# Kernel tuning notes

Measured on AMD Instinct MI355X. Metric: run time of the kernel, lower is better.

## Reference

```python
import jax, jax.numpy as jnp
import numpy as np

N_NODES = 50000
N_EDGES = 600000
IN_DIM = 128
HID = 256
OUT = 3


def setup_inputs() -> dict:
    key = jax.random.key(0)
    ks = jax.random.split(key, 10)
    x = jax.random.normal(ks[0], (N_NODES, IN_DIM), dtype=jnp.float32)
    edge_index = jax.random.randint(ks[1], (2, N_EDGES), 0, N_NODES, dtype=jnp.int64)
    s = lambda k, shp: jax.random.normal(k, shp, dtype=jnp.float32) * (1.0 / np.sqrt(shp[0]))
    return {
        "x": x,
        "edge_index": edge_index,
        # SAGEConv1: lin_l (applied to aggregated neighbors, with bias), lin_r (root, no bias)
        "W1l": s(ks[2], (IN_DIM, HID)), "b1": jnp.zeros((HID,), jnp.float32), "W1r": s(ks[3], (IN_DIM, HID)),
        # SAGEConv2
        "W2l": s(ks[4], (HID, HID)), "b2": jnp.zeros((HID,), jnp.float32), "W2r": s(ks[5], (HID, HID)),
        # classification head
        "Wh": s(ks[6], (HID, OUT)), "bh": jnp.zeros((OUT,), jnp.float32),
    }


def _sage_conv(x, edge_index, Wl, b, Wr):
    """PyG SAGEConv with mean aggregation: out = lin_l(mean_{j->i} x_j) + lin_r(x_i)."""
    src, dst = edge_index[0], edge_index[1]
    n = x.shape[0]
    # gather source features and scatter-mean onto targets
    msg_sum = jax.ops.segment_sum(x[src], dst, num_segments=n)          # [N, d]
    deg = jax.ops.segment_sum(jnp.ones((src.shape[0],), x.dtype), dst, num_segments=n)
    mean = msg_sum / jnp.maximum(deg, 1.0)[:, None]                      # isolated nodes -> 0
    return mean @ Wl + b + x @ Wr


def reference(x, edge_index, W1l, b1, W1r, W2l, b2, W2r, Wh, bh):
    h = jax.nn.relu(_sage_conv(x, edge_index, W1l, b1, W1r))
    # dropout(p=0.2) is identity in eval mode
    h = jax.nn.relu(_sage_conv(h, edge_index, W2l, b2, W2r))
    return h @ Wh + bh
```

## Files before the change

### kernel.cpp

```cpp
#include <hip/hip_runtime.h>
#include <hip/hip_bf16.h>

#define N_NODES 50000
#define N_EDGES 600000
#define IN_DIM 128
#define HID 256
#define OUT_DIM 3

#define M_PAD 50048

#define SCAN_B 256
#define SCAN_NB ((N_NODES + SCAN_B - 1) / SCAN_B)

typedef __bf16 bf16x8 __attribute__((ext_vector_type(8)));
typedef float f32x4 __attribute__((ext_vector_type(4)));

static __device__ __forceinline__ unsigned short f2b(float f) {
    union { float f; unsigned u; } u; u.f = f;
    unsigned r = u.u + 0x7fffu + ((u.u >> 16) & 1u);
    return (unsigned short)(r >> 16);
}
static __device__ __forceinline__ float b2f(unsigned short b) {
    union { unsigned u; float f; } u; u.u = ((unsigned)b) << 16;
    return u.f;
}

static __device__ __forceinline__ size_t swz(int r, int k, int K) {
    return (((size_t)((r >> 4) * (K >> 5) + (k >> 5))) << 9)
         + ((((k >> 3) & 3) * 16 + (r & 15)) << 3) + (k & 7);
}


__global__ void count_deg_kernel(const int* __restrict__ dst, int* __restrict__ counts) {
    int e = blockIdx.x * blockDim.x + threadIdx.x;
    if (e < N_EDGES) atomicAdd(&counts[dst[e]], 1);
}

__global__ __launch_bounds__(256) void block_sum_kernel(const int* __restrict__ counts,
                                                        int* __restrict__ partial) {
    int node = blockIdx.x * SCAN_B + threadIdx.x;
    int v = (node < N_NODES) ? counts[node] : 0;
#pragma unroll
    for (int off = 32; off > 0; off >>= 1) v += __shfl_down(v, off);
    __shared__ int ws[4];
    if ((threadIdx.x & 63) == 0) ws[threadIdx.x >> 6] = v;
    __syncthreads();
    if (threadIdx.x == 0) partial[blockIdx.x] = ws[0] + ws[1] + ws[2] + ws[3];
}

__global__ __launch_bounds__(256) void scan_partial_kernel(int* __restrict__ partial) {
    __shared__ int s[SCAN_B];
    int t = threadIdx.x;
    int v = (t < SCAN_NB) ? partial[t] : 0;
    s[t] = v;
    __syncthreads();
    for (int off = 1; off < SCAN_B; off <<= 1) {
        int u = (t >= off) ? s[t - off] : 0;
        __syncthreads();
        s[t] += u;
        __syncthreads();
    }
    if (t < SCAN_NB) partial[t] = s[t] - v;
}

__global__ __launch_bounds__(256) void write_rowptr_kernel(const int* __restrict__ counts,
                                                           const int* __restrict__ partial,
                                                           int* __restrict__ row_ptr) {
    __shared__ int s[SCAN_B];
    int t = threadIdx.x;
    int node = blockIdx.x * SCAN_B + t;
    int v = (node < N_NODES) ? counts[node] : 0;
    s[t] = v;
    __syncthreads();
    for (int off = 1; off < SCAN_B; off <<= 1) {
        int u = (t >= off) ? s[t - off] : 0;
        __syncthreads();
        s[t] += u;
        __syncthreads();
    }
    if (node < N_NODES) row_ptr[node] = partial[blockIdx.x] + s[t] - v;
    if (node == 0) row_ptr[N_NODES] = N_EDGES;
}

__global__ void fill_csr_kernel(const int* __restrict__ src, const int* __restrict__ dst,
                                const int* __restrict__ row_ptr, int* __restrict__ cursor,
                                int* __restrict__ csr_src) {
    int e = blockIdx.x * blockDim.x + threadIdx.x;
    if (e < N_EDGES) {
        int d = dst[e];
        int pos = atomicAdd(&cursor[d], 1);
        csr_src[row_ptr[d] + pos] = src[e];
    }
}


__global__ void cast_f2b_kernel(const float* __restrict__ in,
                                unsigned short* __restrict__ out_row,
                                unsigned short* __restrict__ out_swz) {
    int i = blockIdx.x * blockDim.x + threadIdx.x;
    if (i * 4 < N_NODES * IN_DIM) {
        float4 v = ((const float4*)in)[i];
        ushort4 o;
        o.x = f2b(v.x); o.y = f2b(v.y); o.z = f2b(v.z); o.w = f2b(v.w);
        ((ushort4*)out_row)[i] = o;
        int m = i >> 5;
        int kb = (i & 31) * 4;
        *(ushort4*)(out_swz + swz(m, kb, IN_DIM)) = o;
    }
}

__global__ void tcast4_kernel(const float* __restrict__ W1l, const float* __restrict__ W1r,
                              const float* __restrict__ W2l, const float* __restrict__ W2r,
                              unsigned short* __restrict__ W1lt, unsigned short* __restrict__ W1rt,
                              unsigned short* __restrict__ W2lt, unsigned short* __restrict__ W2rt) {
    int i = blockIdx.x * blockDim.x + threadIdx.x;
    const float* in; unsigned short* out; int K, base;
    if (i < 32768)        { in = W1l; out = W1lt; K = IN_DIM; base = 0; }
    else if (i < 65536)   { in = W1r; out = W1rt; K = IN_DIM; base = 32768; }
    else if (i < 131072)  { in = W2l; out = W2lt; K = HID;    base = 65536; }
    else if (i < 196608)  { in = W2r; out = W2rt; K = HID;    base = 131072; }
    else return;
    int j = i - base;
    int k = j >> 8;
    int n = j & 255;
    out[swz(n, k, K)] = f2b(in[j]);
}

__global__ void init_out_kernel(const float* __restrict__ bh, float* __restrict__ out) {
    int i = blockIdx.x * blockDim.x + threadIdx.x;
    if (i < N_NODES * 3) out[i] = bh[i % 3];
}


static __device__ __forceinline__ void addv(float* acc, uint4 v) {
    acc[0] += b2f((unsigned short)(v.x & 0xffff));
    acc[1] += b2f((unsigned short)(v.x >> 16));
    acc[2] += b2f((unsigned short)(v.y & 0xffff));
    acc[3] += b2f((unsigned short)(v.y >> 16));
    acc[4] += b2f((unsigned short)(v.z & 0xffff));
    acc[5] += b2f((unsigned short)(v.z >> 16));
    acc[6] += b2f((unsigned short)(v.w & 0xffff));
    acc[7] += b2f((unsigned short)(v.w >> 16));
}

static __device__ __forceinline__ uint4 pack8(const float* a) {
    uint4 pk;
    pk.x = (unsigned)f2b(a[0]) | ((unsigned)f2b(a[1]) << 16);
    pk.y = (unsigned)f2b(a[2]) | ((unsigned)f2b(a[3]) << 16);
    pk.z = (unsigned)f2b(a[4]) | ((unsigned)f2b(a[5]) << 16);
    pk.w = (unsigned)f2b(a[6]) | ((unsigned)f2b(a[7]) << 16);
    return pk;
}

__global__ __launch_bounds__(256) void agg_mean256_kernel(const unsigned short* __restrict__ feat,
                                                          const int* __restrict__ row_ptr,
                                                          const int* __restrict__ csr_src,
                                                          unsigned short* __restrict__ out_swz) {
    int node = blockIdx.x * 4 + (threadIdx.x >> 6);
    if (node >= N_NODES) return;
    int lane = threadIdx.x & 63;
    int half = lane >> 5, lh = lane & 31;
    const uint4* f4 = (const uint4*)feat;
    float acc[8];
#pragma unroll
    for (int j = 0; j < 8; j++) acc[j] = 0.f;
    int beg = row_ptr[node], end = row_ptr[node + 1];
    int i = beg;
    for (; i + 4 <= end; i += 4) {
        int sA = csr_src[i + half];
        int sB = csr_src[i + 2 + half];
        uint4 vA = f4[(size_t)sA * 32 + lh];
        uint4 vB = f4[(size_t)sB * 32 + lh];
        addv(acc, vA);
        addv(acc, vB);
    }
    if (i + 2 <= end) {
        int s = csr_src[i + half];
        addv(acc, f4[(size_t)s * 32 + lh]);
        i += 2;
    }
    if (i < end && half == 0) {
        int s = csr_src[i];
        addv(acc, f4[(size_t)s * 32 + lh]);
    }
    float inv = (end > beg) ? 1.0f / (float)(end - beg) : 0.0f;
#pragma unroll
    for (int j = 0; j < 8; j++) {
        acc[j] += __shfl_xor(acc[j], 32);
        acc[j] *= inv;
    }
    if (half == 0) *(uint4*)(out_swz + swz(node, lh * 8, HID)) = pack8(acc);
}

__global__ __launch_bounds__(256) void agg_mean128_kernel(const unsigned short* __restrict__ feat,
                                                          const int* __restrict__ row_ptr,
                                                          const int* __restrict__ csr_src,
                                                          unsigned short* __restrict__ out_swz) {
    int node = blockIdx.x * 4 + (threadIdx.x >> 6);
    if (node >= N_NODES) return;
    int lane = threadIdx.x & 63;
    int q = lane >> 4, lq = lane & 15;
    const uint4* f4 = (const uint4*)feat;
    float acc[8];
#pragma unroll
    for (int j = 0; j < 8; j++) acc[j] = 0.f;
    int beg = row_ptr[node], end = row_ptr[node + 1];
    int i = beg;
    for (; i + 8 <= end; i += 8) {
        int sA = csr_src[i + q];
        int sB = csr_src[i + 4 + q];
        uint4 vA = f4[(size_t)sA * 16 + lq];
        uint4 vB = f4[(size_t)sB * 16 + lq];
        addv(acc, vA);
        addv(acc, vB);
    }
    if (i + 4 <= end) {
        int s = csr_src[i + q];
        addv(acc, f4[(size_t)s * 16 + lq]);
        i += 4;
    }
    int rem = end - i;
    if (q < rem) {
        int s = csr_src[i + q];
        addv(acc, f4[(size_t)s * 16 + lq]);
    }
    float inv = (end > beg) ? 1.0f / (float)(end - beg) : 0.0f;
#pragma unroll
    for (int j = 0; j < 8; j++) {
        acc[j] += __shfl_xor(acc[j], 32);
        acc[j] += __shfl_xor(acc[j], 16);
        acc[j] *= inv;
    }
    if (q == 0) *(uint4*)(out_swz + swz(node, lq * 8, IN_DIM)) = pack8(acc);
}


template <int K>
static __device__ __forceinline__ void gemm_swz_core(
    const unsigned short* __restrict__ A0, const unsigned short* __restrict__ B0,
    const unsigned short* __restrict__ A1, const unsigned short* __restrict__ B1,
    int tmw, int tn0, int l, f32x4 (&acc)[2][8]) {
    constexpr int KT = K / 32;
    const unsigned short* Ap[2] = {A0, A1};
    const unsigned short* Bp[2] = {B0, B1};
#pragma unroll
    for (int p = 0; p < 2; p++) {
        const unsigned short* A = Ap[p];
        const unsigned short* B = Bp[p];
#pragma unroll
        for (int tk = 0; tk < KT; tk++) {
            bf16x8 a[2], b[8];
            a[0] = *(const bf16x8*)(A + ((((size_t)tmw) * KT + tk) << 9) + l * 8);
            a[1] = *(const bf16x8*)(A + ((((size_t)tmw + 1) * KT + tk) << 9) + l * 8);
#pragma unroll
            for (int nt = 0; nt < 8; nt++)
                b[nt] = *(const bf16x8*)(B + ((((size_t)tn0 + nt) * KT + tk) << 9) + l * 8);
#pragma unroll
            for (int mt = 0; mt < 2; mt++)
#pragma unroll
                for (int nt = 0; nt < 8; nt++)
                    acc[mt][nt] = __builtin_amdgcn_mfma_f32_16x16x32_bf16(a[mt], b[nt],
                                                                          acc[mt][nt], 0, 0, 0);
        }
    }
}

template <int K>
__global__ __launch_bounds__(256, 3) void gemm_swz_kernel(
    const unsigned short* __restrict__ A0, const unsigned short* __restrict__ B0,
    const unsigned short* __restrict__ A1, const unsigned short* __restrict__ B1,
    const float* __restrict__ bias, unsigned short* __restrict__ out_row,
    unsigned short* __restrict__ out_swz, int M) {
    const int t = threadIdx.x;
    const int w = t >> 6, l = t & 63;
    const int quad = l >> 4, lr = l & 15;
    const int m0 = blockIdx.x * 128, n0 = blockIdx.y * 128;
    const int tmw = (m0 >> 4) + w * 2, tn0 = n0 >> 4;

    f32x4 acc[2][8];
    const f32x4 zero = {0.f, 0.f, 0.f, 0.f};
#pragma unroll
    for (int mt = 0; mt < 2; mt++)
#pragma unroll
        for (int nt = 0; nt < 8; nt++) acc[mt][nt] = zero;

    float bias_r[8];
#pragma unroll
    for (int nt = 0; nt < 8; nt++) bias_r[nt] = bias[n0 + nt * 16 + lr];

    gemm_swz_core<K>(A0, B0, A1, B1, tmw, tn0, l, acc);

#pragma unroll
    for (int mt = 0; mt < 2; mt++)
#pragma unroll
        for (int r = 0; r < 4; r++) {
            int gm = m0 + w * 32 + mt * 16 + quad * 4 + r;
            if (gm >= M) continue;
            unsigned short* orow = out_row + (size_t)gm * HID;
#pragma unroll
            for (int nt = 0; nt < 8; nt++) {
                int gn = n0 + nt * 16 + lr;
                unsigned short h = f2b(fmaxf(acc[mt][nt][r] + bias_r[nt], 0.f));
                orow[gn] = h;
                out_swz[swz(gm, gn, HID)] = h;
            }
        }
}

template <int K>
__global__ __launch_bounds__(256, 3) void gemm_swz_head_kernel(
    const unsigned short* __restrict__ A0, const unsigned short* __restrict__ B0,
    const unsigned short* __restrict__ A1, const unsigned short* __restrict__ B1,
    const float* __restrict__ bias, const float* __restrict__ Wh,
    float* __restrict__ out, int M) {
    const int t = threadIdx.x;
    const int w = t >> 6, l = t & 63;
    const int quad = l >> 4, lr = l & 15;
    const int m0 = blockIdx.x * 128, n0 = blockIdx.y * 128;
    const int tmw = (m0 >> 4) + w * 2, tn0 = n0 >> 4;

    f32x4 acc[2][8];
    const f32x4 zero = {0.f, 0.f, 0.f, 0.f};
#pragma unroll
    for (int mt = 0; mt < 2; mt++)
#pragma unroll
        for (int nt = 0; nt < 8; nt++) acc[mt][nt] = zero;

    float bias_r[8];
    float wh_r[8][3];
#pragma unroll
    for (int nt = 0; nt < 8; nt++) {
        int gn = n0 + nt * 16 + lr;
        bias_r[nt] = bias[gn];
        wh_r[nt][0] = Wh[gn * 3 + 0];
        wh_r[nt][1] = Wh[gn * 3 + 1];
        wh_r[nt][2] = Wh[gn * 3 + 2];
    }

    gemm_swz_core<K>(A0, B0, A1, B1, tmw, tn0, l, acc);

#pragma unroll
    for (int mt = 0; mt < 2; mt++)
#pragma unroll
        for (int r = 0; r < 4; r++) {
            int gm = m0 + w * 32 + mt * 16 + quad * 4 + r;
            float p0 = 0.f, p1 = 0.f, p2 = 0.f;
#pragma unroll
            for (int nt = 0; nt < 8; nt++) {
                float v = fmaxf(acc[mt][nt][r] + bias_r[nt], 0.f);
                p0 += v * wh_r[nt][0];
                p1 += v * wh_r[nt][1];
                p2 += v * wh_r[nt][2];
            }
#pragma unroll
            for (int off = 1; off < 16; off <<= 1) {
                p0 += __shfl_xor(p0, off);
                p1 += __shfl_xor(p1, off);
                p2 += __shfl_xor(p2, off);
            }
            if (lr == 0 && gm < M) {
                atomicAdd(&out[(size_t)gm * 3 + 0], p0);
                atomicAdd(&out[(size_t)gm * 3 + 1], p1);
                atomicAdd(&out[(size_t)gm * 3 + 2], p2);
            }
        }
}


extern "C" void kernel_launch(void* const* d_in, const int* in_sizes, int n_in,
                              void* d_out, int out_size, void* d_ws, size_t ws_size,
                              hipStream_t stream) {
    const float* x   = (const float*)d_in[0];
    const int*   ei  = (const int*)d_in[1];
    const int*   src = ei;
    const int*   dst = ei + N_EDGES;
    const float* W1l = (const float*)d_in[2];
    const float* b1  = (const float*)d_in[3];
    const float* W1r = (const float*)d_in[4];
    const float* W2l = (const float*)d_in[5];
    const float* b2  = (const float*)d_in[6];
    const float* W2r = (const float*)d_in[7];
    const float* Wh  = (const float*)d_in[8];
    const float* bh  = (const float*)d_in[9];
    float* out = (float*)d_out;

    char* ws = (char*)d_ws;
    size_t off = 0;
    auto alloc = [&](size_t bytes) -> void* {
        void* p = ws + off;
        off = (off + bytes + 255) & ~(size_t)255;
        return p;
    };
    int* counts   = (int*)alloc((size_t)N_NODES * 4);
    int* row_ptr  = (int*)alloc((size_t)(N_NODES + 1) * 4);
    int* cursor   = (int*)alloc((size_t)N_NODES * 4);
    int* partial  = (int*)alloc((size_t)SCAN_NB * 4);
    int* csr_src  = (int*)alloc((size_t)N_EDGES * 4);
    unsigned short* xb_row  = (unsigned short*)alloc((size_t)M_PAD * IN_DIM * 2);
    unsigned short* xb_swz  = (unsigned short*)alloc((size_t)M_PAD * IN_DIM * 2);
    unsigned short* agg1    = (unsigned short*)alloc((size_t)M_PAD * IN_DIM * 2);
    unsigned short* h1_row  = (unsigned short*)alloc((size_t)M_PAD * HID * 2);
    unsigned short* h1_swz  = (unsigned short*)alloc((size_t)M_PAD * HID * 2);
    unsigned short* agg2    = (unsigned short*)alloc((size_t)M_PAD * HID * 2);
    unsigned short* W1lt = (unsigned short*)alloc((size_t)IN_DIM * HID * 2);
    unsigned short* W1rt = (unsigned short*)alloc((size_t)IN_DIM * HID * 2);
    unsigned short* W2lt = (unsigned short*)alloc((size_t)HID * HID * 2);
    unsigned short* W2rt = (unsigned short*)alloc((size_t)HID * HID * 2);

    hipMemsetAsync(counts, 0, (size_t)N_NODES * 4, stream);
    hipMemsetAsync(cursor, 0, (size_t)N_NODES * 4, stream);

    const int eblocks = (N_EDGES + 255) / 256;
    count_deg_kernel<<<eblocks, 256, 0, stream>>>(dst, counts);
    block_sum_kernel<<<SCAN_NB, SCAN_B, 0, stream>>>(counts, partial);
    scan_partial_kernel<<<1, SCAN_B, 0, stream>>>(partial);
    write_rowptr_kernel<<<SCAN_NB, SCAN_B, 0, stream>>>(counts, partial, row_ptr);
    fill_csr_kernel<<<eblocks, 256, 0, stream>>>(src, dst, row_ptr, cursor, csr_src);

    {
        int n = N_NODES * IN_DIM;
        cast_f2b_kernel<<<(n / 4 + 255) / 256, 256, 0, stream>>>(x, xb_row, xb_swz);
        tcast4_kernel<<<(196608 + 255) / 256, 256, 0, stream>>>(W1l, W1r, W2l, W2r,
                                                                W1lt, W1rt, W2lt, W2rt);
        init_out_kernel<<<(N_NODES * 3 + 255) / 256, 256, 0, stream>>>(bh, out);
    }

    const int nblocks4 = (N_NODES + 3) / 4;
    dim3 gg(M_PAD / 128, 2);

    agg_mean128_kernel<<<nblocks4, 256, 0, stream>>>(xb_row, row_ptr, csr_src, agg1);
    gemm_swz_kernel<IN_DIM><<<gg, 256, 0, stream>>>(agg1, W1lt, xb_swz, W1rt, b1,
                                                    h1_row, h1_swz, N_NODES);

    agg_mean256_kernel<<<nblocks4, 256, 0, stream>>>(h1_row, row_ptr, csr_src, agg2);
    gemm_swz_head_kernel<HID><<<gg, 256, 0, stream>>>(agg2, W2lt, h1_swz, W2rt, b2, Wh,
                                                      out, N_NODES);
}
```

Baseline: 307.9 us.

## Shrink GEMM N-tile to 64, double-buffer register loads, reorder grid for A reuse

Both SAGE GEMM kernels now compute 128x64 output tiles instead of 128x128, which halves the accumulator registers and drops the occupancy hint from launch_bounds. The K loop is flattened across the two operand pairs and software-pipelined: the next k-tile's A/B fragments are loaded into a second register buffer while the MFMAs for the current one run. The grid is transposed so the four N-blocks sharing the same M rows launch next to each other, which should improve L2 reuse of the A tiles. In exchange there are twice as many blocks, each A tile is read four times instead of twice, and the head kernel issues twice as many atomic adds to the output.

```diff
diff --git a/kernel.cpp b/kernel.cpp
--- a/kernel.cpp
+++ b/kernel.cpp
@@ -235,38 +235,44 @@
 }
 
 
-template <int K>
-static __device__ __forceinline__ void gemm_swz_core(
+template <int KP>
+static __device__ __forceinline__ void gemm_swz_core64(
     const unsigned short* __restrict__ A0, const unsigned short* __restrict__ B0,
     const unsigned short* __restrict__ A1, const unsigned short* __restrict__ B1,
-    int tmw, int tn0, int l, f32x4 (&acc)[2][8]) {
-    constexpr int KT = K / 32;
-    const unsigned short* Ap[2] = {A0, A1};
-    const unsigned short* Bp[2] = {B0, B1};
-#pragma unroll
-    for (int p = 0; p < 2; p++) {
-        const unsigned short* A = Ap[p];
-        const unsigned short* B = Bp[p];
-#pragma unroll
-        for (int tk = 0; tk < KT; tk++) {
-            bf16x8 a[2], b[8];
-            a[0] = *(const bf16x8*)(A + ((((size_t)tmw) * KT + tk) << 9) + l * 8);
-            a[1] = *(const bf16x8*)(A + ((((size_t)tmw + 1) * KT + tk) << 9) + l * 8);
-#pragma unroll
-            for (int nt = 0; nt < 8; nt++)
-                b[nt] = *(const bf16x8*)(B + ((((size_t)tn0 + nt) * KT + tk) << 9) + l * 8);
-#pragma unroll
-            for (int mt = 0; mt < 2; mt++)
-#pragma unroll
-                for (int nt = 0; nt < 8; nt++)
-                    acc[mt][nt] = __builtin_amdgcn_mfma_f32_16x16x32_bf16(a[mt], b[nt],
-                                                                          acc[mt][nt], 0, 0, 0);
-        }
-    }
-}
-
-template <int K>
-__global__ __launch_bounds__(256, 3) void gemm_swz_kernel(
+    int tmw, int tn0, int l, f32x4 (&acc)[2][4]) {
+    constexpr int KT = KP / 32;
+    constexpr int TT = 2 * KT;
+    bf16x8 a[2][2], b[2][4];
+
+#define LDTILE(t_, s_)                                                                     \
+    {                                                                                      \
+        const unsigned short* A_ = ((t_) < KT) ? A0 : A1;                                  \
+        const unsigned short* B_ = ((t_) < KT) ? B0 : B1;                                  \
+        const int tk_ = ((t_) < KT) ? (t_) : (t_) - KT;                                    \
+        a[s_][0] = *(const bf16x8*)(A_ + ((((size_t)tmw) * KT + tk_) << 9) + l * 8);       \
+        a[s_][1] = *(const bf16x8*)(A_ + ((((size_t)(tmw + 1)) * KT + tk_) << 9) + l * 8); \
+        _Pragma("unroll")                                                                  \
+        for (int nt = 0; nt < 4; nt++)                                                     \
+            b[s_][nt] = *(const bf16x8*)(B_ + ((((size_t)(tn0 + nt)) * KT + tk_) << 9) + l * 8); \
+    }
+
+    LDTILE(0, 0)
+#pragma unroll
+    for (int t = 0; t < TT; t++) {
+        const int cur = t & 1;
+        if (t + 1 < TT) LDTILE(t + 1, cur ^ 1)
+#pragma unroll
+        for (int mt = 0; mt < 2; mt++)
+#pragma unroll
+            for (int nt = 0; nt < 4; nt++)
+                acc[mt][nt] = __builtin_amdgcn_mfma_f32_16x16x32_bf16(a[cur][mt], b[cur][nt],
+                                                                      acc[mt][nt], 0, 0, 0);
+    }
+#undef LDTILE
+}
+
+template <int KP>
+__global__ __launch_bounds__(256) void gemm_swz_kernel(
     const unsigned short* __restrict__ A0, const unsigned short* __restrict__ B0,
     const unsigned short* __restrict__ A1, const unsigned short* __restrict__ B1,
     const float* __restrict__ bias, unsigned short* __restrict__ out_row,
@@ -274,21 +280,21 @@
     const int t = threadIdx.x;
     const int w = t >> 6, l = t & 63;
     const int quad = l >> 4, lr = l & 15;
-    const int m0 = blockIdx.x * 128, n0 = blockIdx.y * 128;
+    const int n0 = blockIdx.x * 64, m0 = blockIdx.y * 128;
     const int tmw = (m0 >> 4) + w * 2, tn0 = n0 >> 4;
 
-    f32x4 acc[2][8];
+    f32x4 acc[2][4];
     const f32x4 zero = {0.f, 0.f, 0.f, 0.f};
 #pragma unroll
     for (int mt = 0; mt < 2; mt++)
 #pragma unroll
-        for (int nt = 0; nt < 8; nt++) acc[mt][nt] = zero;
-
-    float bias_r[8];
-#pragma unroll
-    for (int nt = 0; nt < 8; nt++) bias_r[nt] = bias[n0 + nt * 16 + lr];
-
-    gemm_swz_core<K>(A0, B0, A1, B1, tmw, tn0, l, acc);
+        for (int nt = 0; nt < 4; nt++) acc[mt][nt] = zero;
+
+    float bias_r[4];
+#pragma unroll
+    for (int nt = 0; nt < 4; nt++) bias_r[nt] = bias[n0 + nt * 16 + lr];
+
+    gemm_swz_core64<KP>(A0, B0, A1, B1, tmw, tn0, l, acc);
 
 #pragma unroll
     for (int mt = 0; mt < 2; mt++)
@@ -298,7 +304,7 @@
             if (gm >= M) continue;
             unsigned short* orow = out_row + (size_t)gm * HID;
 #pragma unroll
-            for (int nt = 0; nt < 8; nt++) {
+            for (int nt = 0; nt < 4; nt++) {
                 int gn = n0 + nt * 16 + lr;
                 unsigned short h = f2b(fmaxf(acc[mt][nt][r] + bias_r[nt], 0.f));
                 orow[gn] = h;
@@ -307,8 +313,8 @@
         }
 }
 
-template <int K>
-__global__ __launch_bounds__(256, 3) void gemm_swz_head_kernel(
+template <int KP>
+__global__ __launch_bounds__(256) void gemm_swz_head_kernel(
     const unsigned short* __restrict__ A0, const unsigned short* __restrict__ B0,
     const unsigned short* __restrict__ A1, const unsigned short* __restrict__ B1,
     const float* __restrict__ bias, const float* __restrict__ Wh,
@@ -316,20 +322,20 @@
     const int t = threadIdx.x;
     const int w = t >> 6, l = t & 63;
     const int quad = l >> 4, lr = l & 15;
-    const int m0 = blockIdx.x * 128, n0 = blockIdx.y * 128;
+    const int n0 = blockIdx.x * 64, m0 = blockIdx.y * 128;
     const int tmw = (m0 >> 4) + w * 2, tn0 = n0 >> 4;
 
-    f32x4 acc[2][8];
+    f32x4 acc[2][4];
     const f32x4 zero = {0.f, 0.f, 0.f, 0.f};
 #pragma unroll
     for (int mt = 0; mt < 2; mt++)
 #pragma unroll
-        for (int nt = 0; nt < 8; nt++) acc[mt][nt] = zero;
-
-    float bias_r[8];
-    float wh_r[8][3];
-#pragma unroll
-    for (int nt = 0; nt < 8; nt++) {
+        for (int nt = 0; nt < 4; nt++) acc[mt][nt] = zero;
+
+    float bias_r[4];
+    float wh_r[4][3];
+#pragma unroll
+    for (int nt = 0; nt < 4; nt++) {
         int gn = n0 + nt * 16 + lr;
         bias_r[nt] = bias[gn];
         wh_r[nt][0] = Wh[gn * 3 + 0];
@@ -337,7 +343,7 @@
         wh_r[nt][2] = Wh[gn * 3 + 2];
     }
 
-    gemm_swz_core<K>(A0, B0, A1, B1, tmw, tn0, l, acc);
+    gemm_swz_core64<KP>(A0, B0, A1, B1, tmw, tn0, l, acc);
 
 #pragma unroll
     for (int mt = 0; mt < 2; mt++)
@@ -346,7 +352,7 @@
             int gm = m0 + w * 32 + mt * 16 + quad * 4 + r;
             float p0 = 0.f, p1 = 0.f, p2 = 0.f;
 #pragma unroll
-            for (int nt = 0; nt < 8; nt++) {
+            for (int nt = 0; nt < 4; nt++) {
                 float v = fmaxf(acc[mt][nt][r] + bias_r[nt], 0.f);
                 p0 += v * wh_r[nt][0];
                 p1 += v * wh_r[nt][1];
@@ -426,7 +432,7 @@
     }
 
     const int nblocks4 = (N_NODES + 3) / 4;
-    dim3 gg(M_PAD / 128, 2);
+    dim3 gg(4, M_PAD / 128);
 
     agg_mean128_kernel<<<nblocks4, 256, 0, stream>>>(xb_row, row_ptr, csr_src, agg1);
     gemm_swz_kernel<IN_DIM><<<gg, 256, 0, stream>>>(agg1, W1lt, xb_swz, W1rt, b1,
```

Measured after the change: 311.9 us. No clear change (+1.3%).
